# Kernel tuning notes

Measured on AMD Instinct MI355X. Metric: run time of the kernel, lower is better.

## Reference

```python
import jax, jax.numpy as jnp
import numpy as np

B, S, D = 2, 2048, 1024
H, DK = 16, 64          # n_heads, d_kv; inner_dim = H*DK = D
NUM_BUCKETS = 32        # T5 relative_attention_num_buckets
MAX_DIST = 128          # T5 relative_attention_max_distance
SM_SCALE = 1.0 / np.sqrt(H)  # module uses 1/sqrt(n_heads), not 1/sqrt(d_kv)


def setup_inputs() -> dict:
    key = jax.random.key(0)
    ks = jax.random.split(key, 6)
    w = 0.02  # typical init scale for projection weights
    return {
        "hidden_states": jax.random.normal(ks[0], (B, S, D), jnp.float32),
        "Wq": jax.random.normal(ks[1], (D, H * DK), jnp.float32) * w,
        "Wk": jax.random.normal(ks[2], (D, H * DK), jnp.float32) * w,
        "Wv": jax.random.normal(ks[3], (D, H * DK), jnp.float32) * w,
        "Wo": jax.random.normal(ks[4], (H * DK, D), jnp.float32) * w,
        "rel_bias": jax.random.normal(ks[5], (NUM_BUCKETS, H), jnp.float32) * w,
    }


def _relative_position_buckets(qlen, klen):
    """T5 bidirectional relative-position bucketing -> [qlen, klen] int32."""
    ctx = jnp.arange(qlen, dtype=jnp.int32)[:, None]
    mem = jnp.arange(klen, dtype=jnp.int32)[None, :]
    rp = mem - ctx  # relative position
    nb = NUM_BUCKETS // 2  # bidirectional split
    ret = (rp > 0).astype(jnp.int32) * nb
    rpa = jnp.abs(rp)
    max_exact = nb // 2
    is_small = rpa < max_exact
    rpf = jnp.maximum(rpa, 1).astype(jnp.float32)
    large = max_exact + (
        jnp.log(rpf / max_exact) / np.log(MAX_DIST / max_exact) * (nb - max_exact)
    ).astype(jnp.int32)
    large = jnp.minimum(large, nb - 1)
    return ret + jnp.where(is_small, rpa, large)


def reference(hidden_states, Wq, Wk, Wv, Wo, rel_bias):
    b, s, d = hidden_states.shape
    q = (hidden_states @ Wq).reshape(b, s, H, DK)
    k = (hidden_states @ Wk).reshape(b, s, H, DK)
    v = (hidden_states @ Wv).reshape(b, s, H, DK)

    buckets = _relative_position_buckets(s, s)        # [S, S]
    bias = rel_bias[buckets]                          # [S, S, H]
    bias = jnp.transpose(bias, (2, 0, 1))[None]       # [1, H, S, S]

    scores = jnp.einsum("bqhd,bkhd->bhqk", q, k) * SM_SCALE + bias
    attn = jax.nn.softmax(scores, axis=-1)
    out = jnp.einsum("bhqk,bkhd->bqhd", attn, v).reshape(b, s, H * DK)
    return out @ Wo
```

## Files before the change

kernel.cpp:

```cpp
#include <hip/hip_runtime.h>
#include <math.h>


typedef _Float16 f16;
typedef _Float16 f16x4 __attribute__((ext_vector_type(4)));
typedef _Float16 f16x8 __attribute__((ext_vector_type(8)));
typedef float f32x4 __attribute__((ext_vector_type(4)));
typedef float f32x16 __attribute__((ext_vector_type(16)));
typedef unsigned int u32;
typedef u32 u32x4 __attribute__((ext_vector_type(4)));

#define MFMA16(a, b, c) __builtin_amdgcn_mfma_f32_16x16x32_f16((a), (b), (c), 0, 0, 0)
#define MFMA32(a, b, c) __builtin_amdgcn_mfma_f32_32x32x16_f16((a), (b), (c), 0, 0, 0)

static __device__ __forceinline__ float EXP2(float x) {
  float r;
  asm("v_exp_f32 %0, %1" : "=v"(r) : "v"(x));
  return r;
}

static __device__ __forceinline__ u32 pk2(float a, float b) {
  return __builtin_bit_cast(u32, __builtin_amdgcn_cvt_pkrtz(a, b));
}
static __device__ __forceinline__ void swap32(u32& a, u32& b) {
  asm volatile("v_permlane32_swap_b32 %0, %1" : "+v"(a), "+v"(b));
}

#define KEEPV8(v8)                                                        \
  do {                                                                    \
    u32x4 _t = __builtin_bit_cast(u32x4, (v8));                           \
    asm volatile("" ::"v"(_t[0]), "v"(_t[1]), "v"(_t[2]), "v"(_t[3]));    \
  } while (0)

__device__ __forceinline__ void gload16(const f16* g, f16* l) {
  __builtin_amdgcn_global_load_lds(
      (const __attribute__((address_space(1))) void*)g,
      (__attribute__((address_space(3))) void*)l, 16, 0, 0);
}


__global__ __launch_bounds__(256) void cast_x_kernel(const float4* __restrict__ x,
                                                     f16x4* __restrict__ xh) {
  int i = blockIdx.x * 256 + threadIdx.x;
  float4 v = x[i];
  f16x4 o;
  o[0] = (f16)v.x; o[1] = (f16)v.y; o[2] = (f16)v.z; o[3] = (f16)v.w;
  xh[i] = o;
}

__global__ void transpose_w_kernel(const float* __restrict__ w0, const float* __restrict__ w1,
                                   const float* __restrict__ w2, const float* __restrict__ w3,
                                   f16* __restrict__ wt) {
  int z = blockIdx.z;
  const float* w = (z == 0) ? w0 : (z == 1) ? w1 : (z == 2) ? w2 : w3;
  float sc = (z == 0) ? 0.36067376022224085f : 1.0f;
  __shared__ float tile[32][33];
  int tx = threadIdx.x, ty = threadIdx.y;
  int kt = blockIdx.x * 32, nt = blockIdx.y * 32;
#pragma unroll
  for (int i = 0; i < 4; ++i)
    tile[ty + i * 8][tx] = w[(size_t)(kt + ty + i * 8) * 1024 + nt + tx];
  __syncthreads();
#pragma unroll
  for (int i = 0; i < 4; ++i)
    wt[((size_t)z * 1024 + nt + ty + i * 8) * 1024 + kt + tx] = (f16)(tile[tx][ty + i * 8] * sc);
}

__global__ __launch_bounds__(256) void bias_kernel(const float* __restrict__ rel_bias,
                                                   f16* __restrict__ bias_rel) {
  int idx = blockIdx.x * 256 + threadIdx.x;
  int h = idx >> 12;
  int r = idx & 4095;
  int rp = r - 2048;
  if (rp < -2047) rp = -2047;
  int bucket = (rp > 0) ? 16 : 0;
  int rpa = (rp < 0) ? -rp : rp;
  if (rpa < 8) {
    bucket += rpa;
  } else {
    int large = 8 + (int)(logf((float)rpa / 8.0f) / logf(16.0f) * 8.0f);
    bucket += (large < 15) ? large : 15;
  }
  bias_rel[idx] = (f16)(rel_bias[bucket * 16 + h] * 1.4426950408889634f);
}

__device__ __forceinline__ void gemm128_core(const f16* __restrict__ A, const f16* __restrict__ Bt,
                                             int mrow, int ncol0, f16* sm ,
                                             f32x4 acc[4][4]) {
  const int t = threadIdx.x;
  const int lane = t & 63, w = t >> 6;
  const int cL = lane & 15, g = lane >> 4;
  const int wr = w >> 1, wc = w & 1;

  const int c0 = w * 128 + lane;
  const int c1 = c0 + 64;
  const int rA0 = c0 >> 2, kA0 = ((c0 & 3) ^ (rA0 & 3)) << 3;
  const int rA1 = c1 >> 2, kA1 = ((c1 & 3) ^ (rA1 & 3)) << 3;
  const f16* gA0 = A + (size_t)(mrow + rA0) * 1024 + kA0;
  const f16* gA1 = A + (size_t)(mrow + rA1) * 1024 + kA1;
  const f16* gB0 = Bt + (size_t)(ncol0 + rA0) * 1024 + kA0;
  const f16* gB1 = Bt + (size_t)(ncol0 + rA1) * 1024 + kA1;
  const int lds0 = (w * 2) * 512, lds1 = (w * 2 + 1) * 512;

#define GSTAGE(buf, k0)                            \
  do {                                             \
    f16* s_ = sm + (buf) * 8192;                   \
    gload16(gA0 + (k0), s_ + lds0);                \
    gload16(gA1 + (k0), s_ + lds1);                \
    gload16(gB0 + (k0), s_ + 4096 + lds0);         \
    gload16(gB1 + (k0), s_ + 4096 + lds1);         \
  } while (0)

  GSTAGE(0, 0);
  __syncthreads();
#pragma unroll 2
  for (int ks = 0; ks < 32; ++ks) {
    const int cur = ks & 1;
    if (ks < 31) GSTAGE(cur ^ 1, (ks + 1) * 32);
    const f16* bA = sm + cur * 8192;
    const f16* bB = bA + 4096;
    f16x8 af[4], bf[4];
#pragma unroll
    for (int m = 0; m < 4; ++m) {
      int r = wr * 64 + m * 16 + cL;
      af[m] = *(const f16x8*)&bA[r * 32 + ((g ^ (r & 3)) << 3)];
    }
#pragma unroll
    for (int n = 0; n < 4; ++n) {
      int r = wc * 64 + n * 16 + cL;
      bf[n] = *(const f16x8*)&bB[r * 32 + ((g ^ (r & 3)) << 3)];
    }
#pragma unroll
    for (int m = 0; m < 4; ++m)
#pragma unroll
      for (int n = 0; n < 4; ++n) acc[m][n] = MFMA16(af[m], bf[n], acc[m][n]);
    __syncthreads();
  }
#undef GSTAGE
}

__global__ __launch_bounds__(256) void gemm_qkv_kernel(const f16* __restrict__ Xh,
                                                       const f16* __restrict__ Wt,
                                                       f16* __restrict__ Qh,
                                                       f16* __restrict__ Kh,
                                                       f16* __restrict__ Vt) {
  __shared__ __align__(16) f16 sm[2][8192];
  int mrow = blockIdx.y * 128, ncol0 = blockIdx.x * 128;
  f32x4 acc[4][4] = {};
  gemm128_core(Xh, Wt, mrow, ncol0, &sm[0][0], acc);
  int lane = threadIdx.x & 63, w = threadIdx.x >> 6;
  int cL = lane & 15, g = lane >> 4;
  int wr = w >> 1, wc = w & 1;
  int which = (ncol0 + wc * 64) >> 10;
#pragma unroll
  for (int m = 0; m < 4; ++m) {
#pragma unroll
    for (int n = 0; n < 4; ++n) {
#pragma unroll
      for (int r = 0; r < 4; ++r) {
        int tt = mrow + wr * 64 + m * 16 + g * 4 + r;
        int b = tt >> 11, s = tt & 2047;
        int col = (ncol0 + wc * 64 + n * 16 + cL) & 1023;
        int hh = col >> 6, dk = col & 63;
        f16 val = (f16)acc[m][n][r];
        if (which == 0)
          Qh[(((size_t)b * 16 + hh) * 2048 + s) * 64 + dk] = val;
        else if (which == 1)
          Kh[(((size_t)b * 16 + hh) * 2048 + s) * 64 + dk] = val;
        else
          Vt[(((size_t)b * 16 + hh) * 64 + dk) * 2048 + s] = val;
      }
    }
  }
}

__global__ __launch_bounds__(256) void gemm_out_kernel(const f16* __restrict__ Oh,
                                                       const f16* __restrict__ WoT,
                                                       float* __restrict__ out) {
  __shared__ __align__(16) f16 sm[2][8192];
  int mrow = blockIdx.y * 128, ncol0 = blockIdx.x * 128;
  f32x4 acc[4][4] = {};
  gemm128_core(Oh, WoT, mrow, ncol0, &sm[0][0], acc);
  int lane = threadIdx.x & 63, w = threadIdx.x >> 6;
  int cL = lane & 15, g = lane >> 4;
  int wr = w >> 1, wc = w & 1;
#pragma unroll
  for (int m = 0; m < 4; ++m)
#pragma unroll
    for (int n = 0; n < 4; ++n)
#pragma unroll
      for (int r = 0; r < 4; ++r) {
        int tt = mrow + wr * 64 + m * 16 + g * 4 + r;
        out[(size_t)tt * 1024 + ncol0 + wc * 64 + n * 16 + cL] = acc[m][n][r];
      }
}

__global__ __launch_bounds__(256) void attn_kernel(const f16* __restrict__ Qh,
                                                   const f16* __restrict__ Kh,
                                                   const f16* __restrict__ Vt,
                                                   const f16* __restrict__ bias_rel,
                                                   f16* __restrict__ Oh) {
  __shared__ __align__(16) f16 sKV[4][8192];
  __shared__ __align__(16) f16 sB[2176];
  const int p = blockIdx.x;
  const int L = ((p & 7) << 6) + (p >> 3);
  const int bh = L >> 4;
  const int qt = (L & 15) << 7;
  const int h = bh & 15, b = bh >> 4;
  int t = threadIdx.x;
  int lane = t & 63, wave = t >> 6;
  int lo5 = lane & 31, hi = lane >> 5;
  const size_t bhS = (size_t)bh * 2048;
  const int qrow = qt + wave * 32 + lo5;

  const f16* qp = Qh + (bhS + qrow) * 64 + hi * 8;
  f16x8 qf[4];
#pragma unroll
  for (int m = 0; m < 4; ++m) qf[m] = *(const f16x8*)(qp + 16 * m);

  float cpos = (float)bias_rel[(size_t)h * 4096 + 4095];
  float cneg = (float)bias_rel[(size_t)h * 4096 + 1];

#pragma unroll
  for (int m = 0; m < 4; ++m) KEEPV8(qf[m]);
  asm volatile("" ::"v"(cpos), "v"(cneg));

  {
    const float4* gB = (const float4*)(bias_rel + (size_t)h * 4096 + 1920 - qt);
    for (int i = t; i < 272; i += 256) ((float4*)sB)[i] = gB[i];
  }

  const int rK0 = t >> 3, ccK0 = ((t & 7) ^ (rK0 & 7)) << 3;
  const int rK1 = rK0 + 32, ccK1 = ((t & 7) ^ (rK1 & 7)) << 3;
  const f16* gK0 = Kh + (bhS + rK0) * 64 + ccK0;
  const f16* gK1 = Kh + (bhS + rK1) * 64 + ccK1;
  const f16* gV0 = Vt + ((size_t)bh * 64 + rK0) * 2048 + ccK0;
  const f16* gV1 = Vt + ((size_t)bh * 64 + rK1) * 2048 + ccK1;
  const int ldsA = wave * 512, ldsB = wave * 512 + 2048;

#define ASTAGE(buf, key0)                           \
  do {                                              \
    f16* s_ = &sKV[buf][0];                         \
    gload16(gK0 + (size_t)(key0) * 64, s_ + ldsA);  \
    gload16(gK1 + (size_t)(key0) * 64, s_ + ldsB);  \
    gload16(gV0 + (key0), s_ + 4096 + ldsA);        \
    gload16(gV1 + (key0), s_ + 4096 + ldsB);        \
  } while (0)

  f32x16 o0 = {}, o1 = {};
  float m_ = -INFINITY, lsum = 0.f;
  const int sw7 = lo5 & 7;

  ASTAGE(0, 0);
  ASTAGE(1, 64);
  asm volatile("s_waitcnt lgkmcnt(0)" ::: "memory");

  for (int kt = 0; kt < 32; ++kt) {
    if (kt < 30) ASTAGE((kt + 2) & 3, (kt + 2) * 64);
    if (kt < 30)
      asm volatile("s_waitcnt vmcnt(8)" ::: "memory");
    else if (kt == 30)
      asm volatile("s_waitcnt vmcnt(4)" ::: "memory");
    else
      asm volatile("s_waitcnt vmcnt(0)" ::: "memory");
    __builtin_amdgcn_s_barrier();

    const int key0 = kt * 64;
    const f16* kb = &sKV[kt & 3][0];
    const f16* vb = kb + 4096;
    const int dkt = key0 - qt;

    f32x16 sa0, sa1;
    if (dkt >= 256 || dkt <= -192) {
      float c = (dkt > 0) ? cpos : cneg;
#pragma unroll
      for (int i = 0; i < 16; ++i) { sa0[i] = c; sa1[i] = c; }
    } else {
      const int bb = key0 + 4 * hi - wave * 32 - lo5 + 128;
#pragma unroll
      for (int i = 0; i < 16; ++i) {
        int pat = (i & 3) + 8 * (i >> 2);
        sa0[i] = (float)sB[bb + pat];
        sa1[i] = (float)sB[bb + 32 + pat];
      }
    }
    const f16* kr0 = kb + lo5 * 64;
    const f16* kr1 = kb + (32 + lo5) * 64;
    __builtin_amdgcn_s_setprio(1);
#pragma unroll
    for (int m = 0; m < 4; ++m) {
      int c = ((2 * m + hi) ^ sw7) << 3;
      sa0 = MFMA32(*(const f16x8*)(kr0 + c), qf[m], sa0);
      sa1 = MFMA32(*(const f16x8*)(kr1 + c), qf[m], sa1);
    }
    __builtin_amdgcn_s_setprio(0);
    float tm[16];
#pragma unroll
    for (int i = 0; i < 16; ++i) tm[i] = fmaxf(sa0[i], sa1[i]);
#pragma unroll
    for (int s2 = 8; s2; s2 >>= 1)
#pragma unroll
      for (int i = 0; i < 8; ++i)
        if (i < s2) tm[i] = fmaxf(tm[i], tm[i + s2]);
    float mx = fmaxf(tm[0], __shfl_xor(tm[0], 32));
    if (__any(mx > m_ + 8.f)) {
      float mn = fmaxf(m_, mx);
      float corr = EXP2(m_ - mn);
      lsum *= corr;
      m_ = mn;
#pragma unroll
      for (int i = 0; i < 16; ++i) { o0[i] *= corr; o1[i] *= corr; }
    }
    float pr[16];
    u32 w0, w1, w2, w3, w4, w5, w6, w7;
#pragma unroll
    for (int i = 0; i < 16; ++i) pr[i] = EXP2(sa0[i] - m_);
    w0 = pk2(pr[0], pr[1]);   w1 = pk2(pr[2], pr[3]);
    w2 = pk2(pr[4], pr[5]);   w3 = pk2(pr[6], pr[7]);
    w4 = pk2(pr[8], pr[9]);   w5 = pk2(pr[10], pr[11]);
    w6 = pk2(pr[12], pr[13]); w7 = pk2(pr[14], pr[15]);
#pragma unroll
    for (int s2 = 8; s2; s2 >>= 1)
#pragma unroll
      for (int i = 0; i < 8; ++i)
        if (i < s2) pr[i] += pr[i + s2];
    float ls = pr[0];
    swap32(w0, w2); swap32(w1, w3); swap32(w4, w6); swap32(w5, w7);
    f16x8 pb0 = __builtin_bit_cast(f16x8, (u32x4){w0, w1, w2, w3});
    f16x8 pb1 = __builtin_bit_cast(f16x8, (u32x4){w4, w5, w6, w7});
#pragma unroll
    for (int i = 0; i < 16; ++i) pr[i] = EXP2(sa1[i] - m_);
    w0 = pk2(pr[0], pr[1]);   w1 = pk2(pr[2], pr[3]);
    w2 = pk2(pr[4], pr[5]);   w3 = pk2(pr[6], pr[7]);
    w4 = pk2(pr[8], pr[9]);   w5 = pk2(pr[10], pr[11]);
    w6 = pk2(pr[12], pr[13]); w7 = pk2(pr[14], pr[15]);
#pragma unroll
    for (int s2 = 8; s2; s2 >>= 1)
#pragma unroll
      for (int i = 0; i < 8; ++i)
        if (i < s2) pr[i] += pr[i + s2];
    lsum += ls + pr[0];
    swap32(w0, w2); swap32(w1, w3); swap32(w4, w6); swap32(w5, w7);
    f16x8 pb2 = __builtin_bit_cast(f16x8, (u32x4){w0, w1, w2, w3});
    f16x8 pb3 = __builtin_bit_cast(f16x8, (u32x4){w4, w5, w6, w7});
    const f16* vr0 = vb + lo5 * 64;
    const f16* vr1 = vb + (32 + lo5) * 64;
    __builtin_amdgcn_s_setprio(1);
    {
      int c = ((0 + hi) ^ sw7) << 3;
      o0 = MFMA32(*(const f16x8*)(vr0 + c), pb0, o0);
      o1 = MFMA32(*(const f16x8*)(vr1 + c), pb0, o1);
    }
    {
      int c = ((2 + hi) ^ sw7) << 3;
      o0 = MFMA32(*(const f16x8*)(vr0 + c), pb1, o0);
      o1 = MFMA32(*(const f16x8*)(vr1 + c), pb1, o1);
    }
    {
      int c = ((4 + hi) ^ sw7) << 3;
      o0 = MFMA32(*(const f16x8*)(vr0 + c), pb2, o0);
      o1 = MFMA32(*(const f16x8*)(vr1 + c), pb2, o1);
    }
    {
      int c = ((6 + hi) ^ sw7) << 3;
      o0 = MFMA32(*(const f16x8*)(vr0 + c), pb3, o0);
      o1 = MFMA32(*(const f16x8*)(vr1 + c), pb3, o1);
    }
    __builtin_amdgcn_s_setprio(0);
  }
#undef ASTAGE
  lsum += __shfl_xor(lsum, 32);
  float inv = 1.0f / lsum;
  size_t base = ((size_t)b * 2048 + qrow) * 1024 + h * 64 + 4 * hi;
#pragma unroll
  for (int rq = 0; rq < 4; ++rq) {
    f16x4 v0, v1;
#pragma unroll
    for (int j = 0; j < 4; ++j) {
      v0[j] = (f16)(o0[rq * 4 + j] * inv);
      v1[j] = (f16)(o1[rq * 4 + j] * inv);
    }
    *(f16x4*)&Oh[base + 8 * rq] = v0;
    *(f16x4*)&Oh[base + 32 + 8 * rq] = v1;
  }
}


extern "C" void kernel_launch(void* const* d_in, const int* in_sizes, int n_in,
                              void* d_out, int out_size, void* d_ws, size_t ws_size,
                              hipStream_t stream) {
  const float* X = (const float*)d_in[0];
  const float* Wq = (const float*)d_in[1];
  const float* Wk = (const float*)d_in[2];
  const float* Wv = (const float*)d_in[3];
  const float* Wo = (const float*)d_in[4];
  const float* relb = (const float*)d_in[5];

  const size_t MB8 = (size_t)8 << 20;
  if (ws_size < 6 * MB8 + (1 << 19)) return;

  char* ws = (char*)d_ws;
  f16* Xh = (f16*)(ws + 0 * MB8);
  f16* Wt = (f16*)(ws + 1 * MB8);
  f16* Qh = (f16*)(ws + 2 * MB8);
  f16* Kh = (f16*)(ws + 3 * MB8);
  f16* Vt = (f16*)(ws + 4 * MB8);
  f16* Oh = (f16*)(ws + 5 * MB8);
  f16* brel = (f16*)(ws + 6 * MB8);

  cast_x_kernel<<<dim3(4096), dim3(256), 0, stream>>>((const float4*)X, (f16x4*)Xh);
  transpose_w_kernel<<<dim3(32, 32, 4), dim3(32, 8), 0, stream>>>(Wq, Wk, Wv, Wo, Wt);
  bias_kernel<<<dim3(256), dim3(256), 0, stream>>>(relb, brel);
  gemm_qkv_kernel<<<dim3(24, 32), dim3(256), 0, stream>>>(Xh, Wt, Qh, Kh, Vt);
  attn_kernel<<<dim3(512), dim3(256), 0, stream>>>(Qh, Kh, Vt, brel, Oh);
  gemm_out_kernel<<<dim3(8, 32), dim3(256), 0, stream>>>(Oh, Wt + (size_t)3072 * 1024,
                                                         (float*)d_out);
}
```

Measured before the change: 148.9 us.

## Process 128 keys per iteration with double-buffered LDS and split accumulators

Restructures the attention loop to handle two 64-key sub-tiles per iteration. Each stage loads 128 keys into one of two double buffers, replacing the four-stage ring of 64-key buffers. The online-softmax max and rescale now run once per 128 keys, and two sets of output accumulators are kept so the PV MFMA chains of the two sub-tiles are independent and summed at the end. This is meant to cut barrier and rescale overhead and give more independent MFMA work to interleave with the exp math. The cost is higher register pressure and a full vmcnt(0) wait at the top of each iteration, so prefetch depth drops from two tiles ahead to one.

```diff
diff --git a/kernel.cpp b/kernel.cpp
--- a/kernel.cpp
+++ b/kernel.cpp
@@ -200,7 +200,7 @@
                                                    const f16* __restrict__ Vt,
                                                    const f16* __restrict__ bias_rel,
                                                    f16* __restrict__ Oh) {
-  __shared__ __align__(16) f16 sKV[4][8192];
+  __shared__ __align__(16) f16 sKV[2][16384];
   __shared__ __align__(16) f16 sB[2176];
   const int p = blockIdx.x;
   const int L = ((p & 7) << 6) + (p >> 3);
@@ -238,137 +238,166 @@
   const f16* gV1 = Vt + ((size_t)bh * 64 + rK1) * 2048 + ccK1;
   const int ldsA = wave * 512, ldsB = wave * 512 + 2048;
 
-#define ASTAGE(buf, key0)                           \
-  do {                                              \
-    f16* s_ = &sKV[buf][0];                         \
-    gload16(gK0 + (size_t)(key0) * 64, s_ + ldsA);  \
-    gload16(gK1 + (size_t)(key0) * 64, s_ + ldsB);  \
-    gload16(gV0 + (key0), s_ + 4096 + ldsA);        \
-    gload16(gV1 + (key0), s_ + 4096 + ldsB);        \
+#define STAGE2(buf, key0)                                      \
+  do {                                                         \
+    f16* s_ = &sKV[buf][0];                                    \
+    gload16(gK0 + (size_t)(key0)*64, s_ + ldsA);               \
+    gload16(gK1 + (size_t)(key0)*64, s_ + ldsB);               \
+    gload16(gV0 + (key0), s_ + 4096 + ldsA);                   \
+    gload16(gV1 + (key0), s_ + 4096 + ldsB);                   \
+    gload16(gK0 + (size_t)(key0 + 64) * 64, s_ + 8192 + ldsA); \
+    gload16(gK1 + (size_t)(key0 + 64) * 64, s_ + 8192 + ldsB); \
+    gload16(gV0 + (key0 + 64), s_ + 12288 + ldsA);             \
+    gload16(gV1 + (key0 + 64), s_ + 12288 + ldsB);             \
   } while (0)
 
-  f32x16 o0 = {}, o1 = {};
+  f32x16 o0A = {}, o1A = {}, o0B = {}, o1B = {};
   float m_ = -INFINITY, lsum = 0.f;
   const int sw7 = lo5 & 7;
 
-  ASTAGE(0, 0);
-  ASTAGE(1, 64);
-  asm volatile("s_waitcnt lgkmcnt(0)" ::: "memory");
-
-  for (int kt = 0; kt < 32; ++kt) {
-    if (kt < 30) ASTAGE((kt + 2) & 3, (kt + 2) * 64);
-    if (kt < 30)
-      asm volatile("s_waitcnt vmcnt(8)" ::: "memory");
-    else if (kt == 30)
-      asm volatile("s_waitcnt vmcnt(4)" ::: "memory");
-    else
-      asm volatile("s_waitcnt vmcnt(0)" ::: "memory");
-    __builtin_amdgcn_s_barrier();
-
-    const int key0 = kt * 64;
-    const f16* kb = &sKV[kt & 3][0];
-    const f16* vb = kb + 4096;
+  auto qk = [&](const f16* kb, f32x16& s0, f32x16& s1) {
+    const f16* kr0 = kb + lo5 * 64;
+    const f16* kr1 = kb + (32 + lo5) * 64;
+#pragma unroll
+    for (int m = 0; m < 4; ++m) {
+      int c = ((2 * m + hi) ^ sw7) << 3;
+      s0 = MFMA32(*(const f16x8*)(kr0 + c), qf[m], s0);
+      s1 = MFMA32(*(const f16x8*)(kr1 + c), qf[m], s1);
+    }
+  };
+  auto rowmax = [&](const f32x16& a, const f32x16& bvec) -> float {
+    float tm[16];
+#pragma unroll
+    for (int i = 0; i < 16; ++i) tm[i] = fmaxf(a[i], bvec[i]);
+#pragma unroll
+    for (int s2 = 8; s2; s2 >>= 1)
+#pragma unroll
+      for (int i = 0; i < 8; ++i)
+        if (i < s2) tm[i] = fmaxf(tm[i], tm[i + s2]);
+    return tm[0];
+  };
+  auto softpack = [&](const f32x16& s0, const f32x16& s1, f16x8& b0, f16x8& b1, f16x8& b2,
+                      f16x8& b3) -> float {
+    float pr[16];
+    u32 w0, w1, w2, w3, w4, w5, w6, w7;
+#pragma unroll
+    for (int i = 0; i < 16; ++i) pr[i] = EXP2(s0[i] - m_);
+    w0 = pk2(pr[0], pr[1]);   w1 = pk2(pr[2], pr[3]);
+    w2 = pk2(pr[4], pr[5]);   w3 = pk2(pr[6], pr[7]);
+    w4 = pk2(pr[8], pr[9]);   w5 = pk2(pr[10], pr[11]);
+    w6 = pk2(pr[12], pr[13]); w7 = pk2(pr[14], pr[15]);
+#pragma unroll
+    for (int s2 = 8; s2; s2 >>= 1)
+#pragma unroll
+      for (int i = 0; i < 8; ++i)
+        if (i < s2) pr[i] += pr[i + s2];
+    float ls = pr[0];
+    swap32(w0, w2); swap32(w1, w3); swap32(w4, w6); swap32(w5, w7);
+    b0 = __builtin_bit_cast(f16x8, (u32x4){w0, w1, w2, w3});
+    b1 = __builtin_bit_cast(f16x8, (u32x4){w4, w5, w6, w7});
+#pragma unroll
+    for (int i = 0; i < 16; ++i) pr[i] = EXP2(s1[i] - m_);
+    w0 = pk2(pr[0], pr[1]);   w1 = pk2(pr[2], pr[3]);
+    w2 = pk2(pr[4], pr[5]);   w3 = pk2(pr[6], pr[7]);
+    w4 = pk2(pr[8], pr[9]);   w5 = pk2(pr[10], pr[11]);
+    w6 = pk2(pr[12], pr[13]); w7 = pk2(pr[14], pr[15]);
+#pragma unroll
+    for (int s2 = 8; s2; s2 >>= 1)
+#pragma unroll
+      for (int i = 0; i < 8; ++i)
+        if (i < s2) pr[i] += pr[i + s2];
+    ls += pr[0];
+    swap32(w0, w2); swap32(w1, w3); swap32(w4, w6); swap32(w5, w7);
+    b2 = __builtin_bit_cast(f16x8, (u32x4){w0, w1, w2, w3});
+    b3 = __builtin_bit_cast(f16x8, (u32x4){w4, w5, w6, w7});
+    return ls;
+  };
+  auto pv = [&](const f16* vb, const f16x8& b0, const f16x8& b1, const f16x8& b2,
+                const f16x8& b3, f32x16& o0, f32x16& o1) {
+    const f16* vr0 = vb + lo5 * 64;
+    const f16* vr1 = vb + (32 + lo5) * 64;
+    {
+      int c = ((0 + hi) ^ sw7) << 3;
+      o0 = MFMA32(*(const f16x8*)(vr0 + c), b0, o0);
+      o1 = MFMA32(*(const f16x8*)(vr1 + c), b0, o1);
+    }
+    {
+      int c = ((2 + hi) ^ sw7) << 3;
+      o0 = MFMA32(*(const f16x8*)(vr0 + c), b1, o0);
+      o1 = MFMA32(*(const f16x8*)(vr1 + c), b1, o1);
+    }
+    {
+      int c = ((4 + hi) ^ sw7) << 3;
+      o0 = MFMA32(*(const f16x8*)(vr0 + c), b2, o0);
+      o1 = MFMA32(*(const f16x8*)(vr1 + c), b2, o1);
+    }
+    {
+      int c = ((6 + hi) ^ sw7) << 3;
+      o0 = MFMA32(*(const f16x8*)(vr0 + c), b3, o0);
+      o1 = MFMA32(*(const f16x8*)(vr1 + c), b3, o1);
+    }
+  };
+  auto biasinit = [&](int key0, f32x16& s0, f32x16& s1) {
     const int dkt = key0 - qt;
-
-    f32x16 sa0, sa1;
     if (dkt >= 256 || dkt <= -192) {
       float c = (dkt > 0) ? cpos : cneg;
 #pragma unroll
-      for (int i = 0; i < 16; ++i) { sa0[i] = c; sa1[i] = c; }
+      for (int i = 0; i < 16; ++i) { s0[i] = c; s1[i] = c; }
     } else {
       const int bb = key0 + 4 * hi - wave * 32 - lo5 + 128;
 #pragma unroll
       for (int i = 0; i < 16; ++i) {
         int pat = (i & 3) + 8 * (i >> 2);
-        sa0[i] = (float)sB[bb + pat];
-        sa1[i] = (float)sB[bb + 32 + pat];
+        s0[i] = (float)sB[bb + pat];
+        s1[i] = (float)sB[bb + 32 + pat];
       }
     }
-    const f16* kr0 = kb + lo5 * 64;
-    const f16* kr1 = kb + (32 + lo5) * 64;
+  };
+
+  STAGE2(0, 0);
+  asm volatile("s_waitcnt lgkmcnt(0)" ::: "memory");
+
+  for (int it = 0; it < 16; ++it) {
+    asm volatile("s_waitcnt vmcnt(0)" ::: "memory");
+    __builtin_amdgcn_s_barrier();
+    if (it < 15) STAGE2((it + 1) & 1, (it + 1) * 128);
+
+    const f16* base = &sKV[it & 1][0];
+    const int key0A = it * 128;
+
+    f32x16 saA0, saA1, saB0, saB1;
+    biasinit(key0A, saA0, saA1);
+    biasinit(key0A + 64, saB0, saB1);
+
     __builtin_amdgcn_s_setprio(1);
-#pragma unroll
-    for (int m = 0; m < 4; ++m) {
-      int c = ((2 * m + hi) ^ sw7) << 3;
-      sa0 = MFMA32(*(const f16x8*)(kr0 + c), qf[m], sa0);
-      sa1 = MFMA32(*(const f16x8*)(kr1 + c), qf[m], sa1);
-    }
+    qk(base, saA0, saA1);
+    qk(base + 8192, saB0, saB1);
     __builtin_amdgcn_s_setprio(0);
-    float tm[16];
-#pragma unroll
-    for (int i = 0; i < 16; ++i) tm[i] = fmaxf(sa0[i], sa1[i]);
-#pragma unroll
-    for (int s2 = 8; s2; s2 >>= 1)
-#pragma unroll
-      for (int i = 0; i < 8; ++i)
-        if (i < s2) tm[i] = fmaxf(tm[i], tm[i + s2]);
-    float mx = fmaxf(tm[0], __shfl_xor(tm[0], 32));
+
+    float mx = fmaxf(rowmax(saA0, saA1), rowmax(saB0, saB1));
+    mx = fmaxf(mx, __shfl_xor(mx, 32));
     if (__any(mx > m_ + 8.f)) {
       float mn = fmaxf(m_, mx);
       float corr = EXP2(m_ - mn);
       lsum *= corr;
       m_ = mn;
 #pragma unroll
-      for (int i = 0; i < 16; ++i) { o0[i] *= corr; o1[i] *= corr; }
-    }
-    float pr[16];
-    u32 w0, w1, w2, w3, w4, w5, w6, w7;
-#pragma unroll
-    for (int i = 0; i < 16; ++i) pr[i] = EXP2(sa0[i] - m_);
-    w0 = pk2(pr[0], pr[1]);   w1 = pk2(pr[2], pr[3]);
-    w2 = pk2(pr[4], pr[5]);   w3 = pk2(pr[6], pr[7]);
-    w4 = pk2(pr[8], pr[9]);   w5 = pk2(pr[10], pr[11]);
-    w6 = pk2(pr[12], pr[13]); w7 = pk2(pr[14], pr[15]);
-#pragma unroll
-    for (int s2 = 8; s2; s2 >>= 1)
-#pragma unroll
-      for (int i = 0; i < 8; ++i)
-        if (i < s2) pr[i] += pr[i + s2];
-    float ls = pr[0];
-    swap32(w0, w2); swap32(w1, w3); swap32(w4, w6); swap32(w5, w7);
-    f16x8 pb0 = __builtin_bit_cast(f16x8, (u32x4){w0, w1, w2, w3});
-    f16x8 pb1 = __builtin_bit_cast(f16x8, (u32x4){w4, w5, w6, w7});
-#pragma unroll
-    for (int i = 0; i < 16; ++i) pr[i] = EXP2(sa1[i] - m_);
-    w0 = pk2(pr[0], pr[1]);   w1 = pk2(pr[2], pr[3]);
-    w2 = pk2(pr[4], pr[5]);   w3 = pk2(pr[6], pr[7]);
-    w4 = pk2(pr[8], pr[9]);   w5 = pk2(pr[10], pr[11]);
-    w6 = pk2(pr[12], pr[13]); w7 = pk2(pr[14], pr[15]);
-#pragma unroll
-    for (int s2 = 8; s2; s2 >>= 1)
-#pragma unroll
-      for (int i = 0; i < 8; ++i)
-        if (i < s2) pr[i] += pr[i + s2];
-    lsum += ls + pr[0];
-    swap32(w0, w2); swap32(w1, w3); swap32(w4, w6); swap32(w5, w7);
-    f16x8 pb2 = __builtin_bit_cast(f16x8, (u32x4){w0, w1, w2, w3});
-    f16x8 pb3 = __builtin_bit_cast(f16x8, (u32x4){w4, w5, w6, w7});
-    const f16* vr0 = vb + lo5 * 64;
-    const f16* vr1 = vb + (32 + lo5) * 64;
+      for (int i = 0; i < 16; ++i) {
+        o0A[i] *= corr; o1A[i] *= corr; o0B[i] *= corr; o1B[i] *= corr;
+      }
+    }
+
+    f16x8 pa0, pa1, pa2, pa3, pb0, pb1, pb2, pb3;
+    lsum += softpack(saA0, saA1, pa0, pa1, pa2, pa3);
     __builtin_amdgcn_s_setprio(1);
-    {
-      int c = ((0 + hi) ^ sw7) << 3;
-      o0 = MFMA32(*(const f16x8*)(vr0 + c), pb0, o0);
-      o1 = MFMA32(*(const f16x8*)(vr1 + c), pb0, o1);
-    }
-    {
-      int c = ((2 + hi) ^ sw7) << 3;
-      o0 = MFMA32(*(const f16x8*)(vr0 + c), pb1, o0);
-      o1 = MFMA32(*(const f16x8*)(vr1 + c), pb1, o1);
-    }
-    {
-      int c = ((4 + hi) ^ sw7) << 3;
-      o0 = MFMA32(*(const f16x8*)(vr0 + c), pb2, o0);
-      o1 = MFMA32(*(const f16x8*)(vr1 + c), pb2, o1);
-    }
-    {
-      int c = ((6 + hi) ^ sw7) << 3;
-      o0 = MFMA32(*(const f16x8*)(vr0 + c), pb3, o0);
-      o1 = MFMA32(*(const f16x8*)(vr1 + c), pb3, o1);
-    }
+    pv(base + 4096, pa0, pa1, pa2, pa3, o0A, o1A);
     __builtin_amdgcn_s_setprio(0);
-  }
-#undef ASTAGE
+    lsum += softpack(saB0, saB1, pb0, pb1, pb2, pb3);
+    __builtin_amdgcn_s_setprio(1);
+    pv(base + 12288, pb0, pb1, pb2, pb3, o0B, o1B);
+    __builtin_amdgcn_s_setprio(0);
+  }
+#undef STAGE2
   lsum += __shfl_xor(lsum, 32);
   float inv = 1.0f / lsum;
   size_t base = ((size_t)b * 2048 + qrow) * 1024 + h * 64 + 4 * hi;
@@ -377,8 +406,8 @@
     f16x4 v0, v1;
 #pragma unroll
     for (int j = 0; j < 4; ++j) {
-      v0[j] = (f16)(o0[rq * 4 + j] * inv);
-      v1[j] = (f16)(o1[rq * 4 + j] * inv);
+      v0[j] = (f16)((o0A[rq * 4 + j] + o0B[rq * 4 + j]) * inv);
+      v1[j] = (f16)((o1A[rq * 4 + j] + o1B[rq * 4 + j]) * inv);
     }
     *(f16x4*)&Oh[base + 8 * rq] = v0;
     *(f16x4*)&Oh[base + 32 + 8 * rq] = v1;
```

Result: slower. 167.7 us (+12.6%).

## Split attention key range across two wave groups with LDS merge

Applied to the files above, without the earlier changes.

Doubles the attention block to 512 threads so two groups of four waves each process half of the key sequence for the same 128 query rows, then merges the partial softmax states (max, sum, output) through shared memory. This raises wave-level parallelism per block and shortens each wave's serial key loop. In exchange the prefetch depth drops from four-stage to double buffering with a full vmcnt(0) wait each iteration, and an extra LDS reduction plus two block barriers are added at the end.

```diff
diff --git a/kernel.cpp b/kernel.cpp
--- a/kernel.cpp
+++ b/kernel.cpp
@@ -195,12 +195,12 @@
       }
 }
 
-__global__ __launch_bounds__(256) void attn_kernel(const f16* __restrict__ Qh,
+__global__ __launch_bounds__(512) void attn_kernel(const f16* __restrict__ Qh,
                                                    const f16* __restrict__ Kh,
                                                    const f16* __restrict__ Vt,
                                                    const f16* __restrict__ bias_rel,
                                                    f16* __restrict__ Oh) {
-  __shared__ __align__(16) f16 sKV[4][8192];
+  __shared__ __align__(16) f16 sKV[2][2][8192];
   __shared__ __align__(16) f16 sB[2176];
   const int p = blockIdx.x;
   const int L = ((p & 7) << 6) + (p >> 3);
@@ -209,9 +209,10 @@
   const int h = bh & 15, b = bh >> 4;
   int t = threadIdx.x;
   int lane = t & 63, wave = t >> 6;
+  const int gr = wave >> 2, sw = wave & 3;
   int lo5 = lane & 31, hi = lane >> 5;
   const size_t bhS = (size_t)bh * 2048;
-  const int qrow = qt + wave * 32 + lo5;
+  const int qrow = qt + sw * 32 + lo5;
 
   const f16* qp = Qh + (bhS + qrow) * 64 + hi * 8;
   f16x8 qf[4];
@@ -227,20 +228,21 @@
 
   {
     const float4* gB = (const float4*)(bias_rel + (size_t)h * 4096 + 1920 - qt);
-    for (int i = t; i < 272; i += 256) ((float4*)sB)[i] = gB[i];
-  }
-
-  const int rK0 = t >> 3, ccK0 = ((t & 7) ^ (rK0 & 7)) << 3;
-  const int rK1 = rK0 + 32, ccK1 = ((t & 7) ^ (rK1 & 7)) << 3;
+    for (int i = t; i < 272; i += 512) ((float4*)sB)[i] = gB[i];
+  }
+
+  const int tg = t & 255;
+  const int rK0 = tg >> 3, ccK0 = ((tg & 7) ^ (rK0 & 7)) << 3;
+  const int rK1 = rK0 + 32, ccK1 = ((tg & 7) ^ (rK1 & 7)) << 3;
   const f16* gK0 = Kh + (bhS + rK0) * 64 + ccK0;
   const f16* gK1 = Kh + (bhS + rK1) * 64 + ccK1;
   const f16* gV0 = Vt + ((size_t)bh * 64 + rK0) * 2048 + ccK0;
   const f16* gV1 = Vt + ((size_t)bh * 64 + rK1) * 2048 + ccK1;
-  const int ldsA = wave * 512, ldsB = wave * 512 + 2048;
+  const int ldsA = sw * 512, ldsB = sw * 512 + 2048;
 
 #define ASTAGE(buf, key0)                           \
   do {                                              \
-    f16* s_ = &sKV[buf][0];                         \
+    f16* s_ = &sKV[gr][buf][0];                     \
     gload16(gK0 + (size_t)(key0) * 64, s_ + ldsA);  \
     gload16(gK1 + (size_t)(key0) * 64, s_ + ldsB);  \
     gload16(gV0 + (key0), s_ + 4096 + ldsA);        \
@@ -250,23 +252,18 @@
   f32x16 o0 = {}, o1 = {};
   float m_ = -INFINITY, lsum = 0.f;
   const int sw7 = lo5 & 7;
-
-  ASTAGE(0, 0);
-  ASTAGE(1, 64);
+  const int kbase = gr << 10;
+
+  ASTAGE(0, kbase);
   asm volatile("s_waitcnt lgkmcnt(0)" ::: "memory");
 
-  for (int kt = 0; kt < 32; ++kt) {
-    if (kt < 30) ASTAGE((kt + 2) & 3, (kt + 2) * 64);
-    if (kt < 30)
-      asm volatile("s_waitcnt vmcnt(8)" ::: "memory");
-    else if (kt == 30)
-      asm volatile("s_waitcnt vmcnt(4)" ::: "memory");
-    else
-      asm volatile("s_waitcnt vmcnt(0)" ::: "memory");
+  for (int it = 0; it < 16; ++it) {
+    asm volatile("s_waitcnt vmcnt(0)" ::: "memory");
     __builtin_amdgcn_s_barrier();
-
-    const int key0 = kt * 64;
-    const f16* kb = &sKV[kt & 3][0];
+    if (it < 15) ASTAGE((it + 1) & 1, kbase + (it + 1) * 64);
+
+    const int key0 = kbase + it * 64;
+    const f16* kb = &sKV[gr][it & 1][0];
     const f16* vb = kb + 4096;
     const int dkt = key0 - qt;
 
@@ -276,7 +273,7 @@
 #pragma unroll
       for (int i = 0; i < 16; ++i) { sa0[i] = c; sa1[i] = c; }
     } else {
-      const int bb = key0 + 4 * hi - wave * 32 - lo5 + 128;
+      const int bb = key0 + 4 * hi - sw * 32 - lo5 + 128;
 #pragma unroll
       for (int i = 0; i < 16; ++i) {
         int pat = (i & 3) + 8 * (i >> 2);
@@ -369,19 +366,39 @@
     __builtin_amdgcn_s_setprio(0);
   }
 #undef ASTAGE
-  lsum += __shfl_xor(lsum, 32);
-  float inv = 1.0f / lsum;
-  size_t base = ((size_t)b * 2048 + qrow) * 1024 + h * 64 + 4 * hi;
-#pragma unroll
-  for (int rq = 0; rq < 4; ++rq) {
-    f16x4 v0, v1;
-#pragma unroll
-    for (int j = 0; j < 4; ++j) {
-      v0[j] = (f16)(o0[rq * 4 + j] * inv);
-      v1[j] = (f16)(o1[rq * 4 + j] * inv);
-    }
-    *(f16x4*)&Oh[base + 8 * rq] = v0;
-    *(f16x4*)&Oh[base + 32 + 8 * rq] = v1;
+
+  __syncthreads();
+  float* sX = (float*)&sKV[0][0][0];
+  const int slot = (sw * 64 + lane) * 35;
+  if (gr == 1) {
+#pragma unroll
+    for (int i = 0; i < 16; ++i) {
+      sX[slot + i] = o0[i];
+      sX[slot + 16 + i] = o1[i];
+    }
+    sX[slot + 32] = m_;
+    sX[slot + 33] = lsum;
+  }
+  __syncthreads();
+  if (gr == 0) {
+    float m2 = sX[slot + 32], l2 = sX[slot + 33];
+    float mn = fmaxf(m_, m2);
+    float c1 = EXP2(m_ - mn), c2 = EXP2(m2 - mn);
+    float s = lsum * c1 + l2 * c2;
+    s += __shfl_xor(s, 32);
+    float inv = 1.0f / s;
+    size_t base = ((size_t)b * 2048 + qrow) * 1024 + h * 64 + 4 * hi;
+#pragma unroll
+    for (int rq = 0; rq < 4; ++rq) {
+      f16x4 v0, v1;
+#pragma unroll
+      for (int j = 0; j < 4; ++j) {
+        v0[j] = (f16)((o0[rq * 4 + j] * c1 + sX[slot + rq * 4 + j] * c2) * inv);
+        v1[j] = (f16)((o1[rq * 4 + j] * c1 + sX[slot + 16 + rq * 4 + j] * c2) * inv);
+      }
+      *(f16x4*)&Oh[base + 8 * rq] = v0;
+      *(f16x4*)&Oh[base + 32 + 8 * rq] = v1;
+    }
   }
 }
 
@@ -412,7 +429,7 @@
   transpose_w_kernel<<<dim3(32, 32, 4), dim3(32, 8), 0, stream>>>(Wq, Wk, Wv, Wo, Wt);
   bias_kernel<<<dim3(256), dim3(256), 0, stream>>>(relb, brel);
   gemm_qkv_kernel<<<dim3(24, 32), dim3(256), 0, stream>>>(Xh, Wt, Qh, Kh, Vt);
-  attn_kernel<<<dim3(512), dim3(256), 0, stream>>>(Qh, Kh, Vt, brel, Oh);
+  attn_kernel<<<dim3(512), dim3(512), 0, stream>>>(Qh, Kh, Vt, brel, Oh);
   gemm_out_kernel<<<dim3(8, 32), dim3(256), 0, stream>>>(Oh, Wt + (size_t)3072 * 1024,
                                                          (float*)d_out);
 }
```

After: 146.6 us. No clear change (-1.5%).
